# Kernel tuning notes

Measured on AMD Instinct MI355X. Metric: run time of the kernel, lower is better.

Reference implementation:

```python
import jax, jax.numpy as jnp
import numpy as np

B, N, U, K = 2, 768, 64, 16
D_IN = 2 * U + K  # 144


def setup_inputs() -> dict:
    key = jax.random.key(0)
    ks = jax.random.split(key, 11)
    s = 1.0 / np.sqrt(D_IN)  # torch Linear-style init scale
    return {
        "seq_embed": jax.random.normal(ks[0], (B, N, U), jnp.float32),
        "rel_encoding": jax.random.normal(ks[1], (N, N, K), jnp.float32),
        "rel_mask": jax.random.randint(ks[2], (N, N), 0, 2, jnp.int32),
        "W1_1": jax.random.uniform(ks[3], (D_IN, D_IN), jnp.float32, -s, s),
        "b1_1": jnp.zeros((D_IN,), jnp.float32),
        "W1_2": jax.random.uniform(ks[4], (D_IN, 1), jnp.float32, -s, s),
        "b1_2": jnp.zeros((1,), jnp.float32),
        "W2_1": jax.random.uniform(ks[5], (D_IN, D_IN), jnp.float32, -s, s),
        "b2_1": jnp.zeros((D_IN,), jnp.float32),
        "W2_2": jax.random.uniform(ks[6], (D_IN, 1), jnp.float32, -s, s),
        "b2_2": jnp.zeros((1,), jnp.float32),
    }


def _forward(seq_embed, rel_encoding, rel_mask, params):
    mask = rel_mask.astype(seq_embed.dtype)[None, :, :, None]  # (1,N,N,1)
    deg = rel_mask.astype(seq_embed.dtype).sum(axis=-1)        # (N,)
    b, n, u = seq_embed.shape
    k = rel_encoding.shape[-1]
    for layers in params:  # one iteration per hop
        e_i = jnp.broadcast_to(seq_embed[:, :, None, :], (b, n, n, u))
        e_j = jnp.broadcast_to(seq_embed[:, None, :, :], (b, n, n, u))
        enc = jnp.broadcast_to(rel_encoding[None], (b, n, n, k))
        combined = jnp.concatenate([e_i, e_j, enc], axis=-1)   # (B,N,N,2U+K)
        h = mask * combined
        for (W, bias) in layers:  # small per-edge MLP, LeakyReLU(0.01)
            h = jax.nn.leaky_relu(h @ W + bias)
        w = (mask * h)[..., 0]                                  # (B,N,N)
        scaled = w / deg[None, :, None]                         # divide by D[i]
        # sum_i scaled[b,i,j] * e_j == seq_embed[b,j] * sum_i scaled[b,i,j]
        s = scaled.sum(axis=1)                                  # (B,N)
        seq_embed = s[..., None] * seq_embed                    # (B,N,U)
    return seq_embed


def reference(seq_embed, rel_encoding, rel_mask, W1_1, b1_1, W1_2, b1_2,
              W2_1, b2_1, W2_2, b2_2):
    params = [((W1_1, b1_1), (W1_2, b1_2)), ((W2_1, b2_1), (W2_2, b2_2))]
    return _forward(seq_embed, rel_encoding, rel_mask, params)
```

## Files before the change

kernel.cpp:

```cpp
#include <hip/hip_runtime.h>

typedef __attribute__((ext_vector_type(8))) short bf16x8;
typedef __attribute__((ext_vector_type(16))) float f32x16;
typedef __attribute__((ext_vector_type(4))) float f32x4;

__device__ inline unsigned short f2bf_rne(float x) {
  unsigned u = __float_as_uint(x);
  unsigned r = u + 0x7FFFu + ((u >> 16) & 1u);
  return (unsigned short)(r >> 16);
}
__device__ inline float bf2f(unsigned short h) {
  return __uint_as_float(((unsigned)h) << 16);
}

__global__ __launch_bounds__(256) void pre_kernel(const float* __restrict__ enc,
                                                  unsigned* __restrict__ encpk,
                                                  const int* __restrict__ mask,
                                                  float* __restrict__ mprep) {
  int bid = blockIdx.x;
  if (bid < 9216) {
    int h = bid * 256 + threadIdx.x;
    f32x4 v = *(const f32x4*)(enc + (size_t)h * 4);
    unsigned lo = (unsigned)f2bf_rne(v[0]) | ((unsigned)f2bf_rne(v[1]) << 16);
    unsigned hi = (unsigned)f2bf_rne(v[2]) | ((unsigned)f2bf_rne(v[3]) << 16);
    uint2 o; o.x = lo; o.y = hi;
    *(uint2*)(encpk + (size_t)h * 2) = o;
  } else {
    int i = bid - 9216, t = threadIdx.x;
    int sum = 0;
    for (int j = t; j < 768; j += 256) sum += mask[i*768 + j];
    for (int off = 32; off; off >>= 1) sum += __shfl_down(sum, off, 64);
    __shared__ int part[4];
    __shared__ float inv_s;
    if ((t & 63) == 0) part[t >> 6] = sum;
    __syncthreads();
    if (t == 0) inv_s = 1.0f / (float)(part[0] + part[1] + part[2] + part[3]);
    __syncthreads();
    float inv = inv_s;
    for (int j = t; j < 768; j += 256) mprep[i*768 + j] = (float)mask[i*768 + j] * inv;
  }
}

template<bool SCALED>
__global__ __launch_bounds__(256) void prep_kernel(const float* __restrict__ seq,
                                                   const float* __restrict__ s_in,
                                                   float* __restrict__ seq_mid,
                                                   const float* __restrict__ W1,
                                                   const float* __restrict__ b1,
                                                   const float* __restrict__ W2,
                                                   unsigned* __restrict__ apk2,
                                                   float* __restrict__ zej,
                                                   unsigned* __restrict__ wpk,
                                                   float* __restrict__ w2pad,
                                                   float* __restrict__ sacc_zero) {
  const int bi0 = blockIdx.x * 16;
  __shared__ float sq[16][64];
  for (int q = threadIdx.x; q < 16*64; q += 256) {
    float v = seq[bi0*64 + q];
    if (SCALED) {
      v *= s_in[bi0 + (q >> 6)];
      seq_mid[bi0*64 + q] = v;
    }
    sq[q >> 6][q & 63] = v;
  }
  __syncthreads();
  const int c = threadIdx.x;
  if (c < 144) {
    float accA[16], accZ[16];
#pragma unroll
    for (int n = 0; n < 16; ++n) { accA[n] = b1[c]; accZ[n] = 0.f; }
#pragma unroll 4
    for (int u = 0; u < 64; ++u) {
      float wa = W1[u*144 + c];
      float wz = W1[(64 + u)*144 + c];
#pragma unroll
      for (int n = 0; n < 16; ++n) {
        float s = sq[n][u];
        accA[n] = fmaf(s, wa, accA[n]);
        accZ[n] = fmaf(s, wz, accZ[n]);
      }
    }
#pragma unroll
    for (int n = 0; n < 16; ++n) {
      int bi = bi0 + n;
      int b = (bi >= 768) ? 1 : 0;
      int nr = bi - b*768;
      unsigned short hi = f2bf_rne(accA[n]);
      unsigned short lo = f2bf_rne(accA[n] - bf2f(hi));
      apk2[(nr*160 + c)*2 + b] = (unsigned)hi | ((unsigned)lo << 16);
      zej[bi*160 + c] = accZ[n];
    }
  } else if (c < 160) {
#pragma unroll
    for (int n = 0; n < 16; ++n) {
      int bi = bi0 + n;
      int b = (bi >= 768) ? 1 : 0;
      int nr = bi - b*768;
      apk2[(nr*160 + c)*2 + b] = 0u;
      zej[bi*160 + c] = 0.f;
    }
  }
  if (blockIdx.x == 0) {
    for (int g = threadIdx.x; g < 1440; g += 256) {
      if (g < 1280) {
        int ew = g & 3;
        int l = (g >> 2) & 63;
        int t = g >> 8;
        int cc = t*32 + (l & 31);
        unsigned short h[2];
#pragma unroll
        for (int q = 0; q < 2; ++q) {
          int e = ew*2 + q;
          int koff = (l >> 5)*8 + e;
          float v = (cc < 144) ? W1[(128 + koff)*144 + cc] : 0.f;
          h[q] = f2bf_rne(v);
        }
        wpk[g] = (unsigned)h[0] | ((unsigned)h[1] << 16);
      } else {
        int cc = g - 1280;
        w2pad[cc] = (cc < 144) ? W2[cc] : 0.f;
      }
    }
  } else if (blockIdx.x == 1) {
    for (int g = threadIdx.x; g < 1536; g += 256) sacc_zero[g] = 0.f;
  }
}

__global__ __launch_bounds__(320, 3) void edge_kernel(
    const unsigned* __restrict__ encpk, const uint2* __restrict__ apkp,
    const float* __restrict__ zej, const unsigned* __restrict__ wpk,
    const float* __restrict__ w2pad, const float* __restrict__ b2p,
    const float* __restrict__ mprep, float* __restrict__ s_out) {
  const int tid = threadIdx.x;
  const int lane = tid & 63;
  const int w = tid >> 6;
  const int jb = blockIdx.x;
  const int i0 = blockIdx.y * 24;
  const int l31 = lane & 31, lh = lane >> 5;
  const int jglob = jb*32 + l31;

  bf16x8 wfrag = ((const bf16x8*)wpk)[w*64 + lane];

  float w2own[16];
#pragma unroll
  for (int r = 0; r < 16; ++r)
    w2own[r] = w2pad[w*32 + (r & 3) + 8*(r >> 2) + 4*lh];

  f32x16 Cz0, Cz1;
#pragma unroll
  for (int q = 0; q < 4; ++q) {
    f32x4 z0 = *(const f32x4*)&zej[(0*768 + jglob)*160 + w*32 + 4*lh + 8*q];
    f32x4 z1 = *(const f32x4*)&zej[(768   + jglob)*160 + w*32 + 4*lh + 8*q];
#pragma unroll
    for (int m = 0; m < 4; ++m) { Cz0[q*4 + m] = z0[m]; Cz1[q*4 + m] = z1[m]; }
  }

  float mp[4][2];
  if (tid < 192) {
    const int j = tid & 31, g6 = tid >> 5;
#pragma unroll
    for (int s = 0; s < 4; ++s) {
      int i1 = i0 + s*6 + (g6 >> 1);
      mp[s][0] = mprep[i1*768 + jb*32 + j];
      mp[s][1] = mprep[(i1 + 3)*768 + jb*32 + j];
    }
  } else {
#pragma unroll
    for (int s = 0; s < 4; ++s) { mp[s][0] = 0.f; mp[s][1] = 0.f; }
  }

  bf16x8 ones;
#pragma unroll
  for (int e = 0; e < 8; ++e) ones[e] = 0;
  if (lh == 0) { ones[0] = (short)0x3F80; ones[1] = (short)0x3F80; }

  __shared__ float pdot[5][2][12][32];
  __shared__ float scomb[192];
  __shared__ __align__(16) char lds_enc[5][4][1024];
  const float b2 = *b2p;

  asm volatile("s_waitcnt vmcnt(0)" ::: "memory");
  __builtin_amdgcn_sched_barrier(0);

  uint2 apkv[4];

#define GLD_ENC(I, SLOT)                                                        \
  __builtin_amdgcn_global_load_lds(                                            \
      (const __attribute__((address_space(1))) unsigned*)(encpk +              \
          (size_t)(i0 + (I))*6144 + jb*256 + l31*8 + lh*4),                     \
      (__attribute__((address_space(3))) unsigned*)&lds_enc[w][SLOT][0], 16, 0, 0)
#define APK(I, SLOT) apkv[SLOT] = apkp[(i0 + (I))*160 + w*32 + l31]

  GLD_ENC(0, 0); APK(0, 0);
  GLD_ENC(1, 1); APK(1, 1);
  GLD_ENC(2, 2); APK(2, 2);

  float sacc_t = 0.f;

  auto body = [&](int unit, int slot) {
    bf16x8 encf = *(const bf16x8*)(&lds_enc[w][slot][lane*16]);
    uint2 av = apkv[slot];

    f32x16 Ce0 = __builtin_amdgcn_mfma_f32_32x32x16_bf16(wfrag, encf, Cz0, 0, 0, 0);
    f32x16 Ce1 = __builtin_amdgcn_mfma_f32_32x32x16_bf16(wfrag, encf, Cz1, 0, 0, 0);

    bf16x8 af0, af1;
#pragma unroll
    for (int e = 2; e < 8; ++e) { af0[e] = 0; af1[e] = 0; }
    *(unsigned*)&af0 = av.x;
    *(unsigned*)&af1 = av.y;

    f32x16 Cb0 = __builtin_amdgcn_mfma_f32_32x32x16_bf16(af0, ones, Ce0, 0, 0, 0);
    f32x16 Cb1 = __builtin_amdgcn_mfma_f32_32x32x16_bf16(af1, ones, Ce1, 0, 0, 0);

    float ta0[2] = {0.f, 0.f}, tb0[2] = {0.f, 0.f};
    float ta1[2] = {0.f, 0.f}, tb1[2] = {0.f, 0.f};
#pragma unroll
    for (int r = 0; r < 16; ++r) {
      float z0 = Cb0[r], z1 = Cb1[r];
      ta0[r & 1] = fmaf(z0, w2own[r], ta0[r & 1]);
      tb0[r & 1] = fmaf(fabsf(z0), w2own[r], tb0[r & 1]);
      ta1[r & 1] = fmaf(z1, w2own[r], ta1[r & 1]);
      tb1[r & 1] = fmaf(fabsf(z1), w2own[r], tb1[r & 1]);
    }
    float dp0 = 0.505f*(ta0[0] + ta0[1]) + 0.495f*(tb0[0] + tb0[1]);
    float dp1 = 0.505f*(ta1[0] + ta1[1]) + 0.495f*(tb1[0] + tb1[1]);
    pdot[w][lh][unit + 0][l31] = dp0;
    pdot[w][lh][unit + 1][l31] = dp1;
  };

#define STEP(IL, VM)                                                            \
  do {                                                                          \
    if ((IL) < 21) { GLD_ENC((IL) + 3, ((IL) + 3) & 3); APK((IL) + 3, ((IL) + 3) & 3); } \
    asm volatile("s_waitcnt vmcnt(" #VM ")" ::: "memory");                      \
    body(((IL) % 6) * 2, (IL) & 3);                                             \
  } while (0)

#define REDUCE(S, LAST)                                                         \
  do {                                                                          \
    asm volatile("s_waitcnt lgkmcnt(0)" ::: "memory");                          \
    __builtin_amdgcn_sched_barrier(0);                                          \
    __builtin_amdgcn_s_barrier();                                               \
    if (tid < 192) {                                                            \
      const int j = tid & 31, g6 = tid >> 5;                                    \
      float s1 = 0.f, s2 = 0.f;                                                 \
      _Pragma("unroll")                                                         \
      for (int w5 = 0; w5 < 5; ++w5) {                                          \
        s1 += pdot[w5][0][g6][j] + pdot[w5][1][g6][j];                          \
        s2 += pdot[w5][0][g6 + 6][j] + pdot[w5][1][g6 + 6][j];                  \
      }                                                                         \
      float wv1 = s1 + b2; wv1 = fmaxf(wv1, 0.01f*wv1);                         \
      float wv2 = s2 + b2; wv2 = fmaxf(wv2, 0.01f*wv2);                         \
      sacc_t = fmaf(mp[S][0], wv1, sacc_t);                                     \
      sacc_t = fmaf(mp[S][1], wv2, sacc_t);                                     \
    }                                                                           \
    if (!(LAST)) {                                                              \
      asm volatile("s_waitcnt lgkmcnt(0)" ::: "memory");                        \
      __builtin_amdgcn_sched_barrier(0);                                        \
      __builtin_amdgcn_s_barrier();                                             \
    }                                                                           \
  } while (0)

  STEP(0, 6);  STEP(1, 6);  STEP(2, 6);  STEP(3, 6);  STEP(4, 6);  STEP(5, 6);
  REDUCE(0, 0);
  STEP(6, 6);  STEP(7, 6);  STEP(8, 6);  STEP(9, 6);  STEP(10, 6); STEP(11, 6);
  REDUCE(1, 0);
  STEP(12, 6); STEP(13, 6); STEP(14, 6); STEP(15, 6); STEP(16, 6); STEP(17, 6);
  REDUCE(2, 0);
  STEP(18, 6); STEP(19, 6); STEP(20, 6); STEP(21, 4); STEP(22, 2); STEP(23, 0);
  REDUCE(3, 1);
#undef STEP
#undef REDUCE
#undef GLD_ENC
#undef APK

  if (tid < 192) scomb[tid] = sacc_t;
  __syncthreads();
  if (tid < 64) {
    const int b = tid >> 5, j = tid & 31;
    float tot = scomb[b*32 + j] + scomb[(b + 2)*32 + j] + scomb[(b + 4)*32 + j];
    atomicAdd(&s_out[b*768 + jb*32 + j], tot);
  }
}

__global__ __launch_bounds__(256) void scale_kernel(const float* __restrict__ s,
                                                    const float* __restrict__ seq_in,
                                                    float* __restrict__ seq_out) {
  int idx = blockIdx.x * 256 + threadIdx.x;
  seq_out[idx] = s[idx >> 6] * seq_in[idx];
}

extern "C" void kernel_launch(void* const* d_in, const int* in_sizes, int n_in,
                              void* d_out, int out_size, void* d_ws, size_t ws_size,
                              hipStream_t stream) {
  const float* seq  = (const float*)d_in[0];
  const float* enc  = (const float*)d_in[1];
  const int*   mask = (const int*)d_in[2];
  const float* W11  = (const float*)d_in[3];
  const float* b11  = (const float*)d_in[4];
  const float* W12  = (const float*)d_in[5];
  const float* b12  = (const float*)d_in[6];
  const float* W21  = (const float*)d_in[7];
  const float* b21  = (const float*)d_in[8];
  const float* W22  = (const float*)d_in[9];
  const float* b22  = (const float*)d_in[10];
  float* out = (float*)d_out;

  float* ws = (float*)d_ws;
  size_t off = 0;
  float* mprep = ws + off;                 off += 768*768;
  unsigned* apk2 = (unsigned*)(ws + off);  off += 2*768*160;
  float* zej = ws + off;                   off += 2*768*160;
  unsigned* wpk = (unsigned*)(ws + off);   off += 1280;
  float* w2pad = ws + off;                 off += 160;
  float* sacc1 = ws + off;                 off += 2*768;
  float* sacc2 = ws + off;                 off += 2*768;
  float* seq_mid = ws + off;               off += 2*768*64;
  unsigned* encpk = (unsigned*)(ws + off); off += 768*768*8;

  pre_kernel<<<9984, 256, 0, stream>>>(enc, encpk, mask, mprep);

  prep_kernel<false><<<96, 256, 0, stream>>>(seq, nullptr, nullptr, W11, b11, W12,
                                             apk2, zej, wpk, w2pad, sacc1);
  edge_kernel<<<dim3(24, 32), 320, 0, stream>>>(encpk, (const uint2*)apk2, zej, wpk,
                                                w2pad, b12, mprep, sacc1);

  prep_kernel<true><<<96, 256, 0, stream>>>(seq, sacc1, seq_mid, W21, b21, W22,
                                            apk2, zej, wpk, w2pad, sacc2);
  edge_kernel<<<dim3(24, 32), 320, 0, stream>>>(encpk, (const uint2*)apk2, zej, wpk,
                                                w2pad, b22, mprep, sacc2);
  scale_kernel<<<384, 256, 0, stream>>>(sacc2, seq_mid, out);
}
```

Measured before the change: 101.6 us.

## Fold linear part of LeakyReLU-W2 dot into extra padded MFMA column

```diff
diff --git a/kernel.cpp b/kernel.cpp
--- a/kernel.cpp
+++ b/kernel.cpp
@@ -55,6 +55,7 @@
                                                    float* __restrict__ sacc_zero) {
   const int bi0 = blockIdx.x * 16;
   __shared__ float sq[16][64];
+  __shared__ float fbuf[16][161];
   for (int q = threadIdx.x; q < 16*64; q += 256) {
     float v = seq[bi0*64 + q];
     if (SCALED) {
@@ -65,8 +66,8 @@
   }
   __syncthreads();
   const int c = threadIdx.x;
+  float accA[16], accZ[16];
   if (c < 144) {
-    float accA[16], accZ[16];
 #pragma unroll
     for (int n = 0; n < 16; ++n) { accA[n] = b1[c]; accZ[n] = 0.f; }
 #pragma unroll 4
@@ -90,7 +91,7 @@
       apk2[(nr*160 + c)*2 + b] = (unsigned)hi | ((unsigned)lo << 16);
       zej[bi*160 + c] = accZ[n];
     }
-  } else if (c < 160) {
+  } else if (c < 160 && c != 144) {
 #pragma unroll
     for (int n = 0; n < 16; ++n) {
       int bi = bi0 + n;
@@ -100,6 +101,35 @@
       zej[bi*160 + c] = 0.f;
     }
   }
+
+  float wc = (c < 144) ? W2[c] : 0.f;
+  if (c < 144) {
+#pragma unroll
+    for (int n = 0; n < 16; ++n) fbuf[n][c] = wc * accA[n];
+  }
+  __syncthreads();
+  if (c < 16) {
+    float s = 0.f;
+    for (int k = 0; k < 144; ++k) s += fbuf[c][k];
+    int bi = bi0 + c;
+    int b = (bi >= 768) ? 1 : 0;
+    int nr = bi - b*768;
+    unsigned short hi = f2bf_rne(s);
+    unsigned short lo = f2bf_rne(s - bf2f(hi));
+    apk2[(nr*160 + 144)*2 + b] = (unsigned)hi | ((unsigned)lo << 16);
+  }
+  __syncthreads();
+  if (c < 144) {
+#pragma unroll
+    for (int n = 0; n < 16; ++n) fbuf[n][c] = wc * accZ[n];
+  }
+  __syncthreads();
+  if (c < 16) {
+    float s = 0.f;
+    for (int k = 0; k < 144; ++k) s += fbuf[c][k];
+    zej[(bi0 + c)*160 + 144] = s;
+  }
+
   if (blockIdx.x == 0) {
     for (int g = threadIdx.x; g < 1440; g += 256) {
       if (g < 1280) {
@@ -112,7 +142,16 @@
         for (int q = 0; q < 2; ++q) {
           int e = ew*2 + q;
           int koff = (l >> 5)*8 + e;
-          float v = (cc < 144) ? W1[(128 + koff)*144 + cc] : 0.f;
+          float v;
+          if (cc < 144) {
+            v = W1[(128 + koff)*144 + cc];
+          } else if (cc == 144) {
+            float s = 0.f;
+            for (int m = 0; m < 144; ++m) s = fmaf(W2[m], W1[(128 + koff)*144 + m], s);
+            v = s;
+          } else {
+            v = 0.f;
+          }
           h[q] = f2bf_rne(v);
         }
         wpk[g] = (unsigned)h[0] | ((unsigned)h[1] << 16);
@@ -213,18 +252,20 @@
     f32x16 Cb0 = __builtin_amdgcn_mfma_f32_32x32x16_bf16(af0, ones, Ce0, 0, 0, 0);
     f32x16 Cb1 = __builtin_amdgcn_mfma_f32_32x32x16_bf16(af1, ones, Ce1, 0, 0, 0);
 
-    float ta0[2] = {0.f, 0.f}, tb0[2] = {0.f, 0.f};
-    float ta1[2] = {0.f, 0.f}, tb1[2] = {0.f, 0.f};
+    float tb0[2] = {0.f, 0.f}, tb1[2] = {0.f, 0.f};
 #pragma unroll
     for (int r = 0; r < 16; ++r) {
-      float z0 = Cb0[r], z1 = Cb1[r];
-      ta0[r & 1] = fmaf(z0, w2own[r], ta0[r & 1]);
-      tb0[r & 1] = fmaf(fabsf(z0), w2own[r], tb0[r & 1]);
-      ta1[r & 1] = fmaf(z1, w2own[r], ta1[r & 1]);
-      tb1[r & 1] = fmaf(fabsf(z1), w2own[r], tb1[r & 1]);
-    }
-    float dp0 = 0.505f*(ta0[0] + ta0[1]) + 0.495f*(tb0[0] + tb0[1]);
-    float dp1 = 0.505f*(ta1[0] + ta1[1]) + 0.495f*(tb1[0] + tb1[1]);
+      tb0[r & 1] = fmaf(fabsf(Cb0[r]), w2own[r], tb0[r & 1]);
+      tb1[r & 1] = fmaf(fabsf(Cb1[r]), w2own[r], tb1[r & 1]);
+    }
+    float dp0 = tb0[0] + tb0[1];
+    float dp1 = tb1[0] + tb1[1];
+    if (w == 4) {
+      if (lh == 0) {
+        dp0 = fmaf(Cb0[8], 1.02020204f, dp0);
+        dp1 = fmaf(Cb1[8], 1.02020204f, dp1);
+      }
+    }
     pdot[w][lh][unit + 0][l31] = dp0;
     pdot[w][lh][unit + 1][l31] = dp1;
   };
@@ -249,8 +290,8 @@
         s1 += pdot[w5][0][g6][j] + pdot[w5][1][g6][j];                          \
         s2 += pdot[w5][0][g6 + 6][j] + pdot[w5][1][g6 + 6][j];                  \
       }                                                                         \
-      float wv1 = s1 + b2; wv1 = fmaxf(wv1, 0.01f*wv1);                         \
-      float wv2 = s2 + b2; wv2 = fmaxf(wv2, 0.01f*wv2);                         \
+      float wv1 = fmaf(s1, 0.495f, b2); wv1 = fmaxf(wv1, 0.01f*wv1);            \
+      float wv2 = fmaf(s2, 0.495f, b2); wv2 = fmaxf(wv2, 0.01f*wv2);            \
       sacc_t = fmaf(mp[S][0], wv1, sacc_t);                                     \
       sacc_t = fmaf(mp[S][1], wv2, sacc_t);                                     \
     }                                                                           \
```

After: 106.6 us. 1.05x slower.
